# Optimization experiments

Measured on AMD Instinct MI355X. Metric: run time of the kernel, lower is better.

The kernel has to match this reference:

```python
import jax, jax.numpy as jnp
import numpy as np

H = 256
LATENT = 128
NODE_FEATS = (12, 5, 4)
EDGE_FEATS = (5, 4)
END_NODE = NODE_FEATS[0] - 1
MAX_NODES = 64


def setup_inputs() -> dict:
    key = jax.random.key(0)
    ks = iter(jax.random.split(key, 40))
    def rn(shape, s=0.1):
        return jax.random.normal(next(ks), shape, dtype=jnp.float32) * s
    inp = {
        "z": jax.random.normal(next(ks), (1, LATENT), dtype=jnp.float32),
        "lp_w": rn((H, LATENT)), "lp_b": rn((H,)),
        "nWih": rn((3 * H, H)), "nWhh": rn((3 * H, H)), "nbih": rn((3 * H,)), "nbhh": rn((3 * H,)),
        "eWih": rn((3 * H, H)), "eWhh": rn((3 * H, H)), "ebih": rn((3 * H,)), "ebhh": rn((3 * H,)),
    }
    for j, f in enumerate(NODE_FEATS):
        inp[f"nc{j}_w"] = rn((f, H)); inp[f"nc{j}_b"] = rn((f,))
    for j, f in enumerate(EDGE_FEATS):
        inp[f"ec{j}_w"] = rn((f, H)); inp[f"ec{j}_b"] = rn((f,))
    inp["max_nodes"] = MAX_NODES
    return inp


def _gru(x, h, Wih, Whh, bih, bhh):
    # torch.nn.GRU single step, single layer. x,h: (1,H)
    gi = x @ Wih.T + bih
    gh = h @ Whh.T + bhh
    ir, iz, inn = jnp.split(gi, 3, axis=-1)
    hr, hz, hn = jnp.split(gh, 3, axis=-1)
    r = jax.nn.sigmoid(ir + hr)
    zg = jax.nn.sigmoid(iz + hz)
    n = jnp.tanh(inn + r * hn)
    return (1.0 - zg) * n + zg * h


def _classify(emb, W, b):
    # Linear -> softmax -> (max prob, argmax), batch=1 -> scalars
    p = jax.nn.softmax(emb @ W.T + b, axis=-1)[0]
    return jnp.max(p), jnp.argmax(p)


def _generate(z, lp_w, lp_b, nWih, nWhh, nbih, nbhh, eWih, eWhh, ebih, ebhh,
              nc0_w, nc0_b, nc1_w, nc1_b, nc2_w, nc2_b,
              ec0_w, ec0_b, ec1_w, ec1_b, max_nodes):
    node_cls = ((nc0_w, nc0_b), (nc1_w, nc1_b), (nc2_w, nc2_b))
    edge_cls = ((ec0_w, ec0_b), (ec1_w, ec1_b))
    h0 = z @ lp_w.T + lp_b                     # latent_project; set_context
    buf0 = jnp.zeros((max_nodes, 1, H), z.dtype)  # node embedding history

    def step(carry, i):
        h, buf, done = carry
        x = jnp.where(i == 0, jnp.zeros((1, H), z.dtype), buf[jnp.maximum(i - 1, 0)])
        h1 = _gru(x, h, nWih, nWhh, nbih, nbhh)   # node_celli.forward_unit; emb = h1
        nps, nis = zip(*[_classify(h1, W, b) for W, b in node_cls])
        nprobs = jnp.stack(nps)                   # (3,)
        nidxs = jnp.stack(nis)                    # (3,) int
        is_end = nidxs[0] == END_NODE

        # edge cell: seq over previous node embeddings, most recent first
        def estep(he, t):
            valid = t < i
            src = jnp.clip(i - 1 - t, 0, max_nodes - 1)
            he2 = _gru(buf[src], he, eWih, eWhh, ebih, ebhh)
            he_new = jnp.where(valid, he2, he)
            eps, eis = zip(*[_classify(he_new, W, b) for W, b in edge_cls])
            return he_new, (jnp.stack(eps), jnp.stack(eis))

        he_fin, (ep_t, ei_t) = jax.lax.scan(estep, h1, jnp.arange(max_nodes))
        # reindex: edge for source node j was produced at inner step t = i-1-j
        js = jnp.arange(max_nodes)
        ts = jnp.clip(i - 1 - js, 0, max_nodes - 1)
        ep_row = ep_t[ts]                          # (max_nodes, 2)
        ei_row = ei_t[ts]
        vj = js < i
        no_edges = jnp.all(jnp.where(vj, ei_row[:, 0] == 0, True)) & (i > 0)

        active = jnp.logical_not(done)
        node_ok = active & jnp.logical_not(is_end) & jnp.logical_not(no_edges)
        done_new = done | is_end | no_edges

        h_next = jnp.where(node_ok & (i > 0), he_fin, h1)  # node hidden <- edge hidden
        h_next = jnp.where(active, h_next, h)
        buf_new = buf.at[i].set(jnp.where(node_ok, h1, buf[i]))

        edge_valid = vj & node_ok & (i > 0)
        out = (jnp.where(node_ok, nprobs, 0.0), nidxs, node_ok,
               jnp.where(edge_valid[:, None], ep_row, 0.0), ei_row, edge_valid)
        return (h_next, buf_new, done_new), out

    _, outs = jax.lax.scan(step, (h0, buf0, jnp.zeros((), bool)), jnp.arange(max_nodes))
    # node_probs (M,3), node_idxs (M,3), node_valid (M,),
    # edge_probs (M,M,2), edge_idxs (M,M,2), edge_valid (M,M)
    return outs


def reference(z, lp_w, lp_b, nWih, nWhh, nbih, nbhh, eWih, eWhh, ebih, ebhh,
              nc0_w, nc0_b, nc1_w, nc1_b, nc2_w, nc2_b,
              ec0_w, ec0_b, ec1_w, ec1_b, max_nodes):
    return _generate(z, lp_w, lp_b, nWih, nWhh, nbih, nbhh, eWih, eWhh, ebih, ebhh,
                     nc0_w, nc0_b, nc1_w, nc1_b, nc2_w, nc2_b,
                     ec0_w, ec0_b, ec1_w, ec1_b, max_nodes)
```

## Files before the change

kernel.cpp:

```cpp
#include <hip/hip_runtime.h>
#include <stdint.h>


#define H 256
#define HL 128
#define G3 768
#define NW 16
#define SL 16
#define MAXN 64
#define NSTATE (1 + MAXN + (MAXN*(MAXN-1))/2)
#define SENTU 0xFFFFFFFFu
#define PAD 264

#define WG_CLS NW
#define WG_HELP0 (NW+1)
#define NHELP_PER 6
#define NWG (WG_HELP0 + 2*NHELP_PER)

#define NP_OFF 0
#define NI_OFF 192
#define NV_OFF 384
#define EP_OFF 448
#define EI_OFF (EP_OFF + MAXN*MAXN*2)
#define EV_OFF (EI_OFF + MAXN*MAXN*2)

struct Wksp {
  float h[NSTATE][H];
  float gi_e[MAXN][G3];
  float gi_n[MAXN][G3];
  unsigned int dec[MAXN];
};

union Shm {
  struct {
    float whe[3*SL*PAD];
    float whn[3*SL*PAD];
    float hcur[H];
    float own[SL];
    float bihe[3*SL], bhhe[3*SL], bihn[3*SL], bhhn[3*SL];
    float zv[HL];
    unsigned int dec;
  } w;
  struct {
    float cw[30*H];
    float cb[30];
    float hc[H];
    float logits[30];
    float resp[5];
    int   resi[5];
    float ept[MAXN][2];
    int   eit[MAXN][2];
  } c;
  struct {
    float h1[H];
  } hp;
};

__device__ __forceinline__ float spinf(const float* p) {
  const unsigned int* u = (const unsigned int*)p;
  unsigned int v = __hip_atomic_load(u, __ATOMIC_RELAXED, __HIP_MEMORY_SCOPE_AGENT);
  while (v == SENTU)
    v = __hip_atomic_load(u, __ATOMIC_RELAXED, __HIP_MEMORY_SCOPE_AGENT);
  return __uint_as_float(v);
}
__device__ __forceinline__ void pubf(float* p, float x) {
  __hip_atomic_store((unsigned int*)p, __float_as_uint(x),
                     __ATOMIC_RELAXED, __HIP_MEMORY_SCOPE_AGENT);
}
__device__ __forceinline__ unsigned int spinu(const unsigned int* p) {
  unsigned int v = __hip_atomic_load(p, __ATOMIC_RELAXED, __HIP_MEMORY_SCOPE_AGENT);
  while (v == SENTU)
    v = __hip_atomic_load(p, __ATOMIC_RELAXED, __HIP_MEMORY_SCOPE_AGENT);
  return v;
}
__device__ __forceinline__ void pubu(unsigned int* p, unsigned int x) {
  __hip_atomic_store(p, x, __ATOMIC_RELAXED, __HIP_MEMORY_SCOPE_AGENT);
}
__device__ __forceinline__ float sigm(float x) { return 1.0f / (1.0f + expf(-x)); }

__global__ __launch_bounds__(256)
void Generator_34746285425383_kernel(
    const float* __restrict__ z, const float* __restrict__ lp_w, const float* __restrict__ lp_b,
    const float* __restrict__ nWih, const float* __restrict__ nWhh,
    const float* __restrict__ nbih, const float* __restrict__ nbhh,
    const float* __restrict__ eWih, const float* __restrict__ eWhh,
    const float* __restrict__ ebih, const float* __restrict__ ebhh,
    const float* __restrict__ nc0w, const float* __restrict__ nc0b,
    const float* __restrict__ nc1w, const float* __restrict__ nc1b,
    const float* __restrict__ nc2w, const float* __restrict__ nc2b,
    const float* __restrict__ ec0w, const float* __restrict__ ec0b,
    const float* __restrict__ ec1w, const float* __restrict__ ec1b,
    float* __restrict__ out, Wksp* __restrict__ ws)
{
  __shared__ Shm S;
  const int bid = blockIdx.x;
  const int tid = threadIdx.x;

  if (bid < NW) {
    const int w = bid, g = tid >> 4, c = tid & 15;
    const int k = w * SL + g;
    for (int r = 0; r < 3 * SL; ++r) {
      const int gate = r / SL, gg = r % SL;
      const int grow = gate * H + (w * SL + gg);
      for (int col = tid; col < H; col += 256) {
        S.w.whe[r * PAD + col] = eWhh[grow * H + col];
        S.w.whn[r * PAD + col] = nWhh[grow * H + col];
      }
    }
    if (tid < 3 * SL) {
      const int gate = tid / SL, gg = tid % SL;
      const int grow = gate * H + w * SL + gg;
      S.w.bihe[tid] = ebih[grow]; S.w.bhhe[tid] = ebhh[grow];
      S.w.bihn[tid] = nbih[grow]; S.w.bhhn[tid] = nbhh[grow];
    }
    if (tid < HL) S.w.zv[tid] = z[tid];
    __syncthreads();

    {
      float p = 0.f;
      for (int it = 0; it < 8; ++it) {
        const int col = c + 16 * it;
        p += S.w.zv[col] * lp_w[k * HL + col];
      }
      for (int off = 1; off < 16; off <<= 1) p += __shfl_xor(p, off);
      const float hp = p + lp_b[k];
      if (c == 0) pubf(&ws->h[0][k], hp);
      if (c == 1) S.w.own[g] = hp;
    }
    __syncthreads();

    int m = 1, idx_carry = 0;
    bool done = false;
    unsigned long long valid = 0ull;
    float pg0 = 0.f, pg1 = 0.f, pg2 = 0.f;
    const float* pga = nullptr;

    for (int i = 0; i < MAXN; ++i) {
      for (int t = -1; t < i; ++t) {
        const bool is_node = (t < 0);
        const int hidx = is_node ? idx_carry : (m - 1);
        const int src  = is_node ? (i - 1) : (i - 1 - t);
        {
          const bool ownfast = (hidx == m - 1) && (tid >= w * SL) && (tid < w * SL + SL);
          const float hv = ownfast ? S.w.own[tid - w * SL] : spinf(&ws->h[hidx][tid]);
          S.w.hcur[tid] = hv;
        }
        float gi0 = 0.f, gi1 = 0.f, gi2 = 0.f;
        const bool use_gi = (src >= 0) && ((valid >> src) & 1ull);
        if (use_gi) {
          gi0 = pg0; gi1 = pg1; gi2 = pg2;
          if (__float_as_uint(gi0) == SENTU) gi0 = spinf(&pga[0 * H + k]);
          if (__float_as_uint(gi1) == SENTU) gi1 = spinf(&pga[1 * H + k]);
          if (__float_as_uint(gi2) == SENTU) gi2 = spinf(&pga[2 * H + k]);
        }
        __syncthreads();
        const float* Wl = is_node ? S.w.whn : S.w.whe;
        float p0 = 0.f, p1 = 0.f, p2 = 0.f;
        #pragma unroll
        for (int it = 0; it < 16; ++it) {
          const int col = c + 16 * it;
          const float hv = S.w.hcur[col];
          p0 += Wl[(0 * SL + g) * PAD + col] * hv;
          p1 += Wl[(1 * SL + g) * PAD + col] * hv;
          p2 += Wl[(2 * SL + g) * PAD + col] * hv;
        }
        for (int off = 1; off < 16; off <<= 1) {
          p0 += __shfl_xor(p0, off);
          p1 += __shfl_xor(p1, off);
          p2 += __shfl_xor(p2, off);
        }
        const float* bih = is_node ? S.w.bihn : S.w.bihe;
        const float* bhh = is_node ? S.w.bhhn : S.w.bhhe;
        const float rr = sigm(gi0 + bih[0 * SL + g] + p0 + bhh[0 * SL + g]);
        const float zz = sigm(gi1 + bih[1 * SL + g] + p1 + bhh[1 * SL + g]);
        const float nn = tanhf(gi2 + bih[2 * SL + g] + rr * (p2 + bhh[2 * SL + g]));
        const float hp = (1.f - zz) * nn + zz * S.w.hcur[k];
        if (c == 0) pubf(&ws->h[m][k], hp);
        if (c == 1) S.w.own[g] = hp;
        {
          int ni = i, nt = t + 1;
          if (nt >= i) { ni = i + 1; nt = -1; }
          if (ni < MAXN) {
            const bool nnode = (nt < 0);
            const int nsrc = nnode ? (ni - 1) : (ni - 1 - nt);
            if (nsrc >= 0) {
              pga = nnode ? ws->gi_n[nsrc] : ws->gi_e[nsrc];
              pg0 = __builtin_nontemporal_load(&pga[0 * H + k]);
              pg1 = __builtin_nontemporal_load(&pga[1 * H + k]);
              pg2 = __builtin_nontemporal_load(&pga[2 * H + k]);
            }
          }
        }
        __syncthreads();
        ++m;
      }
      if (tid == 0) S.w.dec = spinu(&ws->dec[i]);
      __syncthreads();
      const unsigned int dec = S.w.dec;
      const bool is_end   = (dec >> 1) & 1u;
      const bool no_edges = (dec >> 2) & 1u;
      const bool active   = !done;
      const bool node_ok  = active && !is_end && !no_edges;
      if (node_ok) valid |= (1ull << i);
      const int s_end = m - 1, node_m = m - 1 - i;
      if (active) idx_carry = (node_ok && i > 0) ? s_end : node_m;
      done = done || is_end || no_edges;
    }

  } else if (bid == WG_CLS) {
    const int g = tid >> 4, c = tid & 15;
    const float* wsrc[5] = { nc0w, nc1w, nc2w, ec0w, ec1w };
    const float* bsrc[5] = { nc0b, nc1b, nc2b, ec0b, ec1b };
    const int hbase[5] = { 0, 12, 17, 21, 26 };
    const int hlen[5]  = { 12, 5, 4, 5, 4 };
    for (int hh = 0; hh < 5; ++hh)
      for (int r = 0; r < hlen[hh]; ++r)
        for (int col = tid; col < H; col += 256)
          S.c.cw[(hbase[hh] + r) * H + col] = wsrc[hh][r * H + col];
    if (tid < 30) {
      const int hh = tid < 12 ? 0 : tid < 17 ? 1 : tid < 21 ? 2 : tid < 26 ? 3 : 4;
      S.c.cb[tid] = bsrc[hh][tid - hbase[hh]];
    }
    __syncthreads();

    int m = 1;
    bool done = false;
    for (int i = 0; i < MAXN; ++i) {
      float npmax[3]; int nidx[3];
      bool is_end = false, andacc = true;
      for (int t = -1; t < i; ++t) {
        S.c.hc[tid] = spinf(&ws->h[m][tid]);
        __syncthreads();
        for (int rsel = 0; rsel < 2; ++rsel) {
          const int r = g + 16 * rsel;
          float p = 0.f;
          if (r < 30) {
            #pragma unroll
            for (int it = 0; it < 16; ++it) {
              const int col = c + 16 * it;
              p += S.c.cw[r * H + col] * S.c.hc[col];
            }
          }
          for (int off = 1; off < 16; off <<= 1) p += __shfl_xor(p, off);
          if (r < 30 && c == 0) S.c.logits[r] = p + S.c.cb[r];
        }
        __syncthreads();
        if (tid < 5) {
          const int base = hbase[tid], len = hlen[tid];
          float best = S.c.logits[base]; int bi = 0;
          for (int j = 1; j < len; ++j) {
            const float l = S.c.logits[base + j];
            if (l > best) { best = l; bi = j; }
          }
          float s = 0.f;
          for (int j = 0; j < len; ++j) s += expf(S.c.logits[base + j] - best);
          S.c.resp[tid] = 1.0f / s;
          S.c.resi[tid] = bi;
        }
        __syncthreads();
        if (t < 0) {
          npmax[0] = S.c.resp[0]; npmax[1] = S.c.resp[1]; npmax[2] = S.c.resp[2];
          nidx[0] = S.c.resi[0]; nidx[1] = S.c.resi[1]; nidx[2] = S.c.resi[2];
          is_end = (S.c.resi[0] == 11);
          if (i == 0 && tid == 0) {
            S.c.ept[0][0] = S.c.resp[3]; S.c.ept[0][1] = S.c.resp[4];
            S.c.eit[0][0] = S.c.resi[3]; S.c.eit[0][1] = S.c.resi[4];
          }
        } else {
          if (tid == 0) {
            S.c.ept[t][0] = S.c.resp[3]; S.c.ept[t][1] = S.c.resp[4];
            S.c.eit[t][0] = S.c.resi[3]; S.c.eit[t][1] = S.c.resi[4];
          }
          andacc = andacc && (S.c.resi[3] == 0);
        }
        __syncthreads();
        ++m;
      }
      const bool no_edges = (i > 0) && andacc;
      const bool active = !done;
      const bool node_ok = active && !is_end && !no_edges;
      if (tid == 0)
        pubu(&ws->dec[i], 1u | (is_end ? 2u : 0u) | (no_edges ? 4u : 0u));
      if (tid < MAXN) {
        const int j = tid;
        const bool vj = j < i;
        const bool ev = vj && node_ok && (i > 0);
        const int tt = vj ? (i - 1 - j) : 0;
        out[EP_OFF + (i * MAXN + j) * 2 + 0] = ev ? S.c.ept[tt][0] : 0.f;
        out[EP_OFF + (i * MAXN + j) * 2 + 1] = ev ? S.c.ept[tt][1] : 0.f;
        out[EI_OFF + (i * MAXN + j) * 2 + 0] = (float)S.c.eit[tt][0];
        out[EI_OFF + (i * MAXN + j) * 2 + 1] = (float)S.c.eit[tt][1];
        out[EV_OFF + i * MAXN + j] = ev ? 1.f : 0.f;
      } else if (tid < MAXN + 8) {
        const int q = tid - MAXN;
        if (q < 3)       out[NP_OFF + i * 3 + q]       = node_ok ? npmax[q] : 0.f;
        else if (q < 6)  out[NI_OFF + i * 3 + (q - 3)] = (float)nidx[q - 3];
        else if (q == 6) out[NV_OFF + i]               = node_ok ? 1.f : 0.f;
      }
      done = done || is_end || no_edges;
      __syncthreads();
    }

  } else {
    const int e = bid - WG_HELP0;
    const bool is_edge = (e < NHELP_PER);
    const int rowbase = (e % NHELP_PER) * 128;
    const float* Wih = is_edge ? eWih : nWih;
    float* gdst = is_edge ? &ws->gi_e[0][0] : &ws->gi_n[0][0];
    const int g = tid >> 4, c = tid & 15;
    int m_node = 1;
    for (int i = 0; i < MAXN; ++i) {
      S.hp.h1[tid] = spinf(&ws->h[m_node][tid]);
      __syncthreads();
      for (int rr = 0; rr < 8; ++rr) {
        const int row = rowbase + g * 8 + rr;
        float p = 0.f;
        #pragma unroll
        for (int u = 0; u < 4; ++u) {
          const float4 wv = *(const float4*)&Wih[row * H + c * 16 + u * 4];
          p += wv.x * S.hp.h1[c * 16 + u * 4 + 0]
             + wv.y * S.hp.h1[c * 16 + u * 4 + 1]
             + wv.z * S.hp.h1[c * 16 + u * 4 + 2]
             + wv.w * S.hp.h1[c * 16 + u * 4 + 3];
        }
        for (int off = 1; off < 16; off <<= 1) p += __shfl_xor(p, off);
        if (c == 0) pubf(&gdst[i * G3 + row], p);
      }
      __syncthreads();
      m_node += 1 + i;
    }
  }
}

extern "C" void kernel_launch(void* const* d_in, const int* in_sizes, int n_in,
                              void* d_out, int out_size, void* d_ws, size_t ws_size,
                              hipStream_t stream) {
  hipMemsetAsync(d_ws, 0xFF, sizeof(Wksp), stream);
  Generator_34746285425383_kernel<<<dim3(NWG), dim3(256), 0, stream>>>(
      (const float*)d_in[0],  (const float*)d_in[1],  (const float*)d_in[2],
      (const float*)d_in[3],  (const float*)d_in[4],  (const float*)d_in[5],
      (const float*)d_in[6],  (const float*)d_in[7],  (const float*)d_in[8],
      (const float*)d_in[9],  (const float*)d_in[10],
      (const float*)d_in[11], (const float*)d_in[12],
      (const float*)d_in[13], (const float*)d_in[14],
      (const float*)d_in[15], (const float*)d_in[16],
      (const float*)d_in[17], (const float*)d_in[18],
      (const float*)d_in[19], (const float*)d_in[20],
      (float*)d_out, (Wksp*)d_ws);
}
```

Before: 5.216 ms.

## Fold classifier into every GRU workgroup, dropping the cross-block decision handshake

```diff
diff --git a/kernel.cpp b/kernel.cpp
--- a/kernel.cpp
+++ b/kernel.cpp
@@ -11,11 +11,8 @@
 #define NSTATE (1 + MAXN + (MAXN*(MAXN-1))/2)
 #define SENTU 0xFFFFFFFFu
 #define PAD 264
-
-#define WG_CLS NW
-#define WG_HELP0 (NW+1)
-#define NHELP_PER 6
-#define NWG (WG_HELP0 + 2*NHELP_PER)
+#define NHELP 4
+#define NWG (NW + NHELP)
 
 #define NP_OFF 0
 #define NI_OFF 192
@@ -28,32 +25,27 @@
   float h[NSTATE][H];
   float gi_e[MAXN][G3];
   float gi_n[MAXN][G3];
-  unsigned int dec[MAXN];
 };
 
 union Shm {
   struct {
     float whe[3*SL*PAD];
     float whn[3*SL*PAD];
-    float hcur[H];
+    float cw[30*PAD];
+    float hg[H];
+    float h1s[H];
+    float hkeep[H];
     float own[SL];
     float bihe[3*SL], bhhe[3*SL], bihn[3*SL], bhhn[3*SL];
+    float cb[30];
     float zv[HL];
-    unsigned int dec;
+    float logits[30];
+    float np[3];  int ni[3];
+    float ep0[MAXN], ep1[MAXN];
+    int   ei0[MAXN], ei1[MAXN];
+    unsigned int isend, andflag;
   } w;
-  struct {
-    float cw[30*H];
-    float cb[30];
-    float hc[H];
-    float logits[30];
-    float resp[5];
-    int   resi[5];
-    float ept[MAXN][2];
-    int   eit[MAXN][2];
-  } c;
-  struct {
-    float h1[H];
-  } hp;
+  struct { float h1[H]; } hp;
 };
 
 __device__ __forceinline__ float spinf(const float* p) {
@@ -63,18 +55,18 @@
     v = __hip_atomic_load(u, __ATOMIC_RELAXED, __HIP_MEMORY_SCOPE_AGENT);
   return __uint_as_float(v);
 }
+__device__ __forceinline__ float spinf_slow(const float* p) {
+  const unsigned int* u = (const unsigned int*)p;
+  unsigned int v = __hip_atomic_load(u, __ATOMIC_RELAXED, __HIP_MEMORY_SCOPE_AGENT);
+  while (v == SENTU) {
+    __builtin_amdgcn_s_sleep(1);
+    v = __hip_atomic_load(u, __ATOMIC_RELAXED, __HIP_MEMORY_SCOPE_AGENT);
+  }
+  return __uint_as_float(v);
+}
 __device__ __forceinline__ void pubf(float* p, float x) {
   __hip_atomic_store((unsigned int*)p, __float_as_uint(x),
                      __ATOMIC_RELAXED, __HIP_MEMORY_SCOPE_AGENT);
-}
-__device__ __forceinline__ unsigned int spinu(const unsigned int* p) {
-  unsigned int v = __hip_atomic_load(p, __ATOMIC_RELAXED, __HIP_MEMORY_SCOPE_AGENT);
-  while (v == SENTU)
-    v = __hip_atomic_load(p, __ATOMIC_RELAXED, __HIP_MEMORY_SCOPE_AGENT);
-  return v;
-}
-__device__ __forceinline__ void pubu(unsigned int* p, unsigned int x) {
-  __hip_atomic_store(p, x, __ATOMIC_RELAXED, __HIP_MEMORY_SCOPE_AGENT);
 }
 __device__ __forceinline__ float sigm(float x) { return 1.0f / (1.0f + expf(-x)); }
 
@@ -107,6 +99,20 @@
         S.w.whn[r * PAD + col] = nWhh[grow * H + col];
       }
     }
+    {
+      const float* wsrc[5] = { nc0w, nc1w, nc2w, ec0w, ec1w };
+      const float* bsrc[5] = { nc0b, nc1b, nc2b, ec0b, ec1b };
+      const int hbase[5] = { 0, 12, 17, 21, 26 };
+      const int hlen[5]  = { 12, 5, 4, 5, 4 };
+      for (int hh = 0; hh < 5; ++hh)
+        for (int r = 0; r < hlen[hh]; ++r)
+          for (int col = tid; col < H; col += 256)
+            S.w.cw[(hbase[hh] + r) * PAD + col] = wsrc[hh][r * H + col];
+      if (tid < 30) {
+        const int hh = tid < 12 ? 0 : tid < 17 ? 1 : tid < 21 ? 2 : tid < 26 ? 3 : 4;
+        S.w.cb[tid] = bsrc[hh][tid - hbase[hh]];
+      }
+    }
     if (tid < 3 * SL) {
       const int gate = tid / SL, gg = tid % SL;
       const int grow = gate * H + w * SL + gg;
@@ -114,6 +120,7 @@
       S.w.bihn[tid] = nbih[grow]; S.w.bhhn[tid] = nbhh[grow];
     }
     if (tid < HL) S.w.zv[tid] = z[tid];
+    if (tid == 0) { S.w.andflag = 1u; S.w.isend = 0u; }
     __syncthreads();
 
     {
@@ -129,7 +136,7 @@
     }
     __syncthreads();
 
-    int m = 1, idx_carry = 0;
+    int m = 1;
     bool done = false;
     unsigned long long valid = 0ull;
     float pg0 = 0.f, pg1 = 0.f, pg2 = 0.f;
@@ -138,13 +145,87 @@
     for (int i = 0; i < MAXN; ++i) {
       for (int t = -1; t < i; ++t) {
         const bool is_node = (t < 0);
-        const int hidx = is_node ? idx_carry : (m - 1);
-        const int src  = is_node ? (i - 1) : (i - 1 - t);
+        float* dst = (t == 0) ? S.w.h1s : S.w.hg;
         {
-          const bool ownfast = (hidx == m - 1) && (tid >= w * SL) && (tid < w * SL + SL);
-          const float hv = ownfast ? S.w.own[tid - w * SL] : spinf(&ws->h[hidx][tid]);
-          S.w.hcur[tid] = hv;
-        }
+          const bool ownfast = (tid >= w * SL) && (tid < w * SL + SL);
+          dst[tid] = ownfast ? S.w.own[tid - w * SL] : spinf(&ws->h[m - 1][tid]);
+        }
+        __syncthreads();
+        const bool do_cls = !(is_node && i == 0);
+        if (do_cls) {
+          for (int rsel = 0; rsel < 2; ++rsel) {
+            const int r = g + 16 * rsel;
+            float p = 0.f;
+            if (r < 30) {
+              #pragma unroll
+              for (int it = 0; it < 16; ++it) {
+                const int col = c + 16 * it;
+                p += S.w.cw[r * PAD + col] * dst[col];
+              }
+            }
+            for (int off = 1; off < 16; off <<= 1) p += __shfl_xor(p, off);
+            if (r < 30 && c == 0) S.w.logits[r] = p + S.w.cb[r];
+          }
+        }
+        if (is_node && i > 0) {
+          const int r_ = i - 1;
+          __syncthreads();
+          if (tid < 5) {
+            const int base = tid == 0 ? 0 : tid == 1 ? 12 : tid == 2 ? 17 : tid == 3 ? 21 : 26;
+            const int len  = tid == 0 ? 12 : tid == 1 ? 5 : tid == 2 ? 4 : tid == 3 ? 5 : 4;
+            float best = S.w.logits[base]; int bi = 0;
+            for (int j = 1; j < len; ++j) {
+              const float l = S.w.logits[base + j];
+              if (l > best) { best = l; bi = j; }
+            }
+            float s = 0.f;
+            for (int j = 0; j < len; ++j) s += expf(S.w.logits[base + j] - best);
+            const float pm = 1.0f / s;
+            if (r_ == 0) {
+              if (tid < 3) { S.w.np[tid] = pm; S.w.ni[tid] = bi;
+                             if (tid == 0) S.w.isend = (bi == 11) ? 1u : 0u; }
+              if (tid == 3) { S.w.ep0[0] = pm; S.w.ei0[0] = bi; }
+              if (tid == 4) { S.w.ep1[0] = pm; S.w.ei1[0] = bi; }
+            } else {
+              if (tid == 3) { S.w.ep0[r_ - 1] = pm; S.w.ei0[r_ - 1] = bi;
+                              if (bi != 0) S.w.andflag = 0u; }
+              if (tid == 4) { S.w.ep1[r_ - 1] = pm; S.w.ei1[r_ - 1] = bi; }
+            }
+          }
+          __syncthreads();
+          const bool is_end   = S.w.isend != 0u;
+          const bool no_edges = (r_ > 0) && (S.w.andflag != 0u);
+          const bool active   = !done;
+          const bool node_ok  = active && !is_end && !no_edges;
+          if (node_ok) valid |= (1ull << r_);
+          if (w == 0) {
+            if (tid < MAXN) {
+              const int j = tid;
+              const bool vj = j < r_;
+              const bool ev = vj && node_ok && (r_ > 0);
+              const int tt = vj ? (r_ - 1 - j) : 0;
+              out[EP_OFF + (r_ * MAXN + j) * 2 + 0] = ev ? S.w.ep0[tt] : 0.f;
+              out[EP_OFF + (r_ * MAXN + j) * 2 + 1] = ev ? S.w.ep1[tt] : 0.f;
+              out[EI_OFF + (r_ * MAXN + j) * 2 + 0] = (float)S.w.ei0[tt];
+              out[EI_OFF + (r_ * MAXN + j) * 2 + 1] = (float)S.w.ei1[tt];
+              out[EV_OFF + r_ * MAXN + j] = ev ? 1.f : 0.f;
+            } else if (tid < MAXN + 8) {
+              const int q = tid - MAXN;
+              if (q < 3)       out[NP_OFF + r_ * 3 + q]       = node_ok ? S.w.np[q] : 0.f;
+              else if (q < 6)  out[NI_OFF + r_ * 3 + (q - 3)] = (float)S.w.ni[q - 3];
+              else if (q == 6) out[NV_OFF + r_]               = node_ok ? 1.f : 0.f;
+            }
+          }
+          if (active) {
+            const bool useg = (node_ok && r_ > 0) || (r_ == 0);
+            S.w.hkeep[tid] = useg ? S.w.hg[tid] : S.w.h1s[tid];
+          }
+          done = done || is_end || no_edges;
+          __syncthreads();
+          if (tid == 0) S.w.andflag = 1u;
+        }
+        const float* hb = is_node ? (i == 0 ? S.w.hg : S.w.hkeep) : dst;
+        const int src = is_node ? (i - 1) : (i - 1 - t);
         float gi0 = 0.f, gi1 = 0.f, gi2 = 0.f;
         const bool use_gi = (src >= 0) && ((valid >> src) & 1ull);
         if (use_gi) {
@@ -153,13 +234,12 @@
           if (__float_as_uint(gi1) == SENTU) gi1 = spinf(&pga[1 * H + k]);
           if (__float_as_uint(gi2) == SENTU) gi2 = spinf(&pga[2 * H + k]);
         }
-        __syncthreads();
         const float* Wl = is_node ? S.w.whn : S.w.whe;
         float p0 = 0.f, p1 = 0.f, p2 = 0.f;
         #pragma unroll
         for (int it = 0; it < 16; ++it) {
           const int col = c + 16 * it;
-          const float hv = S.w.hcur[col];
+          const float hv = hb[col];
           p0 += Wl[(0 * SL + g) * PAD + col] * hv;
           p1 += Wl[(1 * SL + g) * PAD + col] * hv;
           p2 += Wl[(2 * SL + g) * PAD + col] * hv;
@@ -174,15 +254,15 @@
         const float rr = sigm(gi0 + bih[0 * SL + g] + p0 + bhh[0 * SL + g]);
         const float zz = sigm(gi1 + bih[1 * SL + g] + p1 + bhh[1 * SL + g]);
         const float nn = tanhf(gi2 + bih[2 * SL + g] + rr * (p2 + bhh[2 * SL + g]));
-        const float hp = (1.f - zz) * nn + zz * S.w.hcur[k];
+        const float hp = (1.f - zz) * nn + zz * hb[k];
         if (c == 0) pubf(&ws->h[m][k], hp);
         if (c == 1) S.w.own[g] = hp;
         {
-          int ni = i, nt = t + 1;
-          if (nt >= i) { ni = i + 1; nt = -1; }
-          if (ni < MAXN) {
-            const bool nnode = (nt < 0);
-            const int nsrc = nnode ? (ni - 1) : (ni - 1 - nt);
+          int ni_ = i, nt_ = t + 1;
+          if (nt_ >= i) { ni_ = i + 1; nt_ = -1; }
+          if (ni_ < MAXN) {
+            const bool nnode = (nt_ < 0);
+            const int nsrc = nnode ? (ni_ - 1) : (ni_ - 1 - nt_);
             if (nsrc >= 0) {
               pga = nnode ? ws->gi_n[nsrc] : ws->gi_e[nsrc];
               pg0 = __builtin_nontemporal_load(&pga[0 * H + k]);
@@ -192,128 +272,105 @@
           }
         }
         __syncthreads();
+        if (!is_node && tid < 5) {
+          const int base = tid == 0 ? 0 : tid == 1 ? 12 : tid == 2 ? 17 : tid == 3 ? 21 : 26;
+          const int len  = tid == 0 ? 12 : tid == 1 ? 5 : tid == 2 ? 4 : tid == 3 ? 5 : 4;
+          float best = S.w.logits[base]; int bi = 0;
+          for (int j = 1; j < len; ++j) {
+            const float l = S.w.logits[base + j];
+            if (l > best) { best = l; bi = j; }
+          }
+          float s = 0.f;
+          for (int j = 0; j < len; ++j) s += expf(S.w.logits[base + j] - best);
+          const float pm = 1.0f / s;
+          if (t == 0) {
+            if (tid < 3) { S.w.np[tid] = pm; S.w.ni[tid] = bi;
+                           if (tid == 0) S.w.isend = (bi == 11) ? 1u : 0u; }
+          } else {
+            if (tid == 3) { S.w.ep0[t - 1] = pm; S.w.ei0[t - 1] = bi;
+                            if (bi != 0) S.w.andflag = 0u; }
+            if (tid == 4) { S.w.ep1[t - 1] = pm; S.w.ei1[t - 1] = bi; }
+          }
+        }
         ++m;
       }
-      if (tid == 0) S.w.dec = spinu(&ws->dec[i]);
+    }
+
+    {
+      const int r_ = MAXN - 1;
+      float* dst = S.w.hg;
+      {
+        const bool ownfast = (tid >= w * SL) && (tid < w * SL + SL);
+        dst[tid] = ownfast ? S.w.own[tid - w * SL] : spinf(&ws->h[NSTATE - 1][tid]);
+      }
       __syncthreads();
-      const unsigned int dec = S.w.dec;
-      const bool is_end   = (dec >> 1) & 1u;
-      const bool no_edges = (dec >> 2) & 1u;
-      const bool active   = !done;
-      const bool node_ok  = active && !is_end && !no_edges;
-      if (node_ok) valid |= (1ull << i);
-      const int s_end = m - 1, node_m = m - 1 - i;
-      if (active) idx_carry = (node_ok && i > 0) ? s_end : node_m;
-      done = done || is_end || no_edges;
-    }
-
-  } else if (bid == WG_CLS) {
-    const int g = tid >> 4, c = tid & 15;
-    const float* wsrc[5] = { nc0w, nc1w, nc2w, ec0w, ec1w };
-    const float* bsrc[5] = { nc0b, nc1b, nc2b, ec0b, ec1b };
-    const int hbase[5] = { 0, 12, 17, 21, 26 };
-    const int hlen[5]  = { 12, 5, 4, 5, 4 };
-    for (int hh = 0; hh < 5; ++hh)
-      for (int r = 0; r < hlen[hh]; ++r)
-        for (int col = tid; col < H; col += 256)
-          S.c.cw[(hbase[hh] + r) * H + col] = wsrc[hh][r * H + col];
-    if (tid < 30) {
-      const int hh = tid < 12 ? 0 : tid < 17 ? 1 : tid < 21 ? 2 : tid < 26 ? 3 : 4;
-      S.c.cb[tid] = bsrc[hh][tid - hbase[hh]];
-    }
-    __syncthreads();
-
-    int m = 1;
-    bool done = false;
-    for (int i = 0; i < MAXN; ++i) {
-      float npmax[3]; int nidx[3];
-      bool is_end = false, andacc = true;
-      for (int t = -1; t < i; ++t) {
-        S.c.hc[tid] = spinf(&ws->h[m][tid]);
-        __syncthreads();
-        for (int rsel = 0; rsel < 2; ++rsel) {
-          const int r = g + 16 * rsel;
-          float p = 0.f;
-          if (r < 30) {
-            #pragma unroll
-            for (int it = 0; it < 16; ++it) {
-              const int col = c + 16 * it;
-              p += S.c.cw[r * H + col] * S.c.hc[col];
-            }
-          }
-          for (int off = 1; off < 16; off <<= 1) p += __shfl_xor(p, off);
-          if (r < 30 && c == 0) S.c.logits[r] = p + S.c.cb[r];
-        }
-        __syncthreads();
-        if (tid < 5) {
-          const int base = hbase[tid], len = hlen[tid];
-          float best = S.c.logits[base]; int bi = 0;
-          for (int j = 1; j < len; ++j) {
-            const float l = S.c.logits[base + j];
-            if (l > best) { best = l; bi = j; }
-          }
-          float s = 0.f;
-          for (int j = 0; j < len; ++j) s += expf(S.c.logits[base + j] - best);
-          S.c.resp[tid] = 1.0f / s;
-          S.c.resi[tid] = bi;
-        }
-        __syncthreads();
-        if (t < 0) {
-          npmax[0] = S.c.resp[0]; npmax[1] = S.c.resp[1]; npmax[2] = S.c.resp[2];
-          nidx[0] = S.c.resi[0]; nidx[1] = S.c.resi[1]; nidx[2] = S.c.resi[2];
-          is_end = (S.c.resi[0] == 11);
-          if (i == 0 && tid == 0) {
-            S.c.ept[0][0] = S.c.resp[3]; S.c.ept[0][1] = S.c.resp[4];
-            S.c.eit[0][0] = S.c.resi[3]; S.c.eit[0][1] = S.c.resi[4];
-          }
-        } else {
-          if (tid == 0) {
-            S.c.ept[t][0] = S.c.resp[3]; S.c.ept[t][1] = S.c.resp[4];
-            S.c.eit[t][0] = S.c.resi[3]; S.c.eit[t][1] = S.c.resi[4];
-          }
-          andacc = andacc && (S.c.resi[3] == 0);
-        }
-        __syncthreads();
-        ++m;
-      }
-      const bool no_edges = (i > 0) && andacc;
-      const bool active = !done;
-      const bool node_ok = active && !is_end && !no_edges;
-      if (tid == 0)
-        pubu(&ws->dec[i], 1u | (is_end ? 2u : 0u) | (no_edges ? 4u : 0u));
-      if (tid < MAXN) {
-        const int j = tid;
-        const bool vj = j < i;
-        const bool ev = vj && node_ok && (i > 0);
-        const int tt = vj ? (i - 1 - j) : 0;
-        out[EP_OFF + (i * MAXN + j) * 2 + 0] = ev ? S.c.ept[tt][0] : 0.f;
-        out[EP_OFF + (i * MAXN + j) * 2 + 1] = ev ? S.c.ept[tt][1] : 0.f;
-        out[EI_OFF + (i * MAXN + j) * 2 + 0] = (float)S.c.eit[tt][0];
-        out[EI_OFF + (i * MAXN + j) * 2 + 1] = (float)S.c.eit[tt][1];
-        out[EV_OFF + i * MAXN + j] = ev ? 1.f : 0.f;
-      } else if (tid < MAXN + 8) {
-        const int q = tid - MAXN;
-        if (q < 3)       out[NP_OFF + i * 3 + q]       = node_ok ? npmax[q] : 0.f;
-        else if (q < 6)  out[NI_OFF + i * 3 + (q - 3)] = (float)nidx[q - 3];
-        else if (q == 6) out[NV_OFF + i]               = node_ok ? 1.f : 0.f;
-      }
-      done = done || is_end || no_edges;
+      for (int rsel = 0; rsel < 2; ++rsel) {
+        const int r = g + 16 * rsel;
+        float p = 0.f;
+        if (r < 30) {
+          #pragma unroll
+          for (int it = 0; it < 16; ++it) {
+            const int col = c + 16 * it;
+            p += S.w.cw[r * PAD + col] * dst[col];
+          }
+        }
+        for (int off = 1; off < 16; off <<= 1) p += __shfl_xor(p, off);
+        if (r < 30 && c == 0) S.w.logits[r] = p + S.w.cb[r];
+      }
       __syncthreads();
+      if (tid < 5) {
+        const int base = tid == 0 ? 0 : tid == 1 ? 12 : tid == 2 ? 17 : tid == 3 ? 21 : 26;
+        const int len  = tid == 0 ? 12 : tid == 1 ? 5 : tid == 2 ? 4 : tid == 3 ? 5 : 4;
+        float best = S.w.logits[base]; int bi = 0;
+        for (int j = 1; j < len; ++j) {
+          const float l = S.w.logits[base + j];
+          if (l > best) { best = l; bi = j; }
+        }
+        float s = 0.f;
+        for (int j = 0; j < len; ++j) s += expf(S.w.logits[base + j] - best);
+        const float pm = 1.0f / s;
+        if (tid == 3) { S.w.ep0[r_ - 1] = pm; S.w.ei0[r_ - 1] = bi;
+                        if (bi != 0) S.w.andflag = 0u; }
+        if (tid == 4) { S.w.ep1[r_ - 1] = pm; S.w.ei1[r_ - 1] = bi; }
+      }
+      __syncthreads();
+      if (w == 0) {
+        const bool is_end   = S.w.isend != 0u;
+        const bool no_edges = S.w.andflag != 0u;
+        const bool active   = !done;
+        const bool node_ok  = active && !is_end && !no_edges;
+        if (tid < MAXN) {
+          const int j = tid;
+          const bool vj = j < r_;
+          const bool ev = vj && node_ok;
+          const int tt = vj ? (r_ - 1 - j) : 0;
+          out[EP_OFF + (r_ * MAXN + j) * 2 + 0] = ev ? S.w.ep0[tt] : 0.f;
+          out[EP_OFF + (r_ * MAXN + j) * 2 + 1] = ev ? S.w.ep1[tt] : 0.f;
+          out[EI_OFF + (r_ * MAXN + j) * 2 + 0] = (float)S.w.ei0[tt];
+          out[EI_OFF + (r_ * MAXN + j) * 2 + 1] = (float)S.w.ei1[tt];
+          out[EV_OFF + r_ * MAXN + j] = ev ? 1.f : 0.f;
+        } else if (tid < MAXN + 8) {
+          const int q = tid - MAXN;
+          if (q < 3)       out[NP_OFF + r_ * 3 + q]       = node_ok ? S.w.np[q] : 0.f;
+          else if (q < 6)  out[NI_OFF + r_ * 3 + (q - 3)] = (float)S.w.ni[q - 3];
+          else if (q == 6) out[NV_OFF + r_]               = node_ok ? 1.f : 0.f;
+        }
+      }
     }
 
   } else {
-    const int e = bid - WG_HELP0;
-    const bool is_edge = (e < NHELP_PER);
-    const int rowbase = (e % NHELP_PER) * 128;
+    const int e = bid - NW;
+    const bool is_edge = (e < 2);
+    const int rowbase = (e & 1) * 384;
     const float* Wih = is_edge ? eWih : nWih;
     float* gdst = is_edge ? &ws->gi_e[0][0] : &ws->gi_n[0][0];
     const int g = tid >> 4, c = tid & 15;
     int m_node = 1;
     for (int i = 0; i < MAXN; ++i) {
-      S.hp.h1[tid] = spinf(&ws->h[m_node][tid]);
+      S.hp.h1[tid] = spinf_slow(&ws->h[m_node][tid]);
       __syncthreads();
-      for (int rr = 0; rr < 8; ++rr) {
-        const int row = rowbase + g * 8 + rr;
+      for (int rr = 0; rr < 24; ++rr) {
+        const int row = rowbase + g * 24 + rr;
         float p = 0.f;
         #pragma unroll
         for (int u = 0; u < 4; ++u) {
```

Result: slower. 7.668 ms (+47.0%).
